# Performance work log

Measured on AMD Instinct MI355X. Metric: run time of the kernel, lower is better.

Reference implementation:

```python
import jax, jax.numpy as jnp
import numpy as np

HIDDEN = 768
HEADS = 12
HEAD_DIM = HIDDEN // HEADS


def setup_inputs() -> dict:
    key = jax.random.key(0)
    ks = jax.random.split(key, 5)
    B, S = 1, 4096
    scale = 1.0 / np.sqrt(HIDDEN)
    return {
        "x": jax.random.normal(ks[0], (B, S, HIDDEN), dtype=jnp.float32),
        "w_qkv": jax.random.normal(ks[1], (HIDDEN, 3 * HIDDEN), dtype=jnp.float32) * scale,
        "b_qkv": jnp.zeros((3 * HIDDEN,), dtype=jnp.float32),
        "w_proj": jax.random.normal(ks[2], (HIDDEN, HIDDEN), dtype=jnp.float32) * scale,
        "b_proj": jnp.zeros((HIDDEN,), dtype=jnp.float32),
    }


def reference(x, w_qkv, b_qkv, w_proj, b_proj):
    B, S, D = x.shape
    H, Hd = HEADS, HEAD_DIM
    qkv = x @ w_qkv + b_qkv                        # [B,S,3D]
    qkv = qkv.reshape(B, S, 3, H, Hd)
    q, k, v = (jnp.moveaxis(qkv[:, :, i], 2, 1) for i in range(3))  # [B,H,S,Hd]
    scale = 1.0 / np.sqrt(Hd)
    attn = jnp.einsum("bhqd,bhkd->bhqk", q, k) * scale
    attn = jax.nn.softmax(attn, axis=-1)
    o = jnp.einsum("bhqk,bhkd->bhqd", attn, v)     # [B,H,S,Hd]
    o = jnp.moveaxis(o, 1, 2).reshape(B, S, D)
    return o @ w_proj + b_proj
```

## Files before the change

kernel.cpp:

```cpp
#include <hip/hip_runtime.h>

#define S_LEN 4096
#define DMODEL 768
#define NHEAD 12
#define HDIM 64
#define DQKV 2304

typedef __attribute__((ext_vector_type(8))) __bf16 bf16x8;
typedef __attribute__((ext_vector_type(4))) float f32x4;
typedef __attribute__((ext_vector_type(8))) unsigned short ushort8;

#define LOG2E 1.4426950408889634f

#if __has_builtin(__builtin_amdgcn_exp2f)
#define EXP2(x) __builtin_amdgcn_exp2f(x)
#else
#define EXP2(x) exp2f(x)
#endif

static __device__ __forceinline__ unsigned short f2bf(float f) {
  unsigned int u = __float_as_uint(f);
  u += 0x7FFFu + ((u >> 16) & 1u);
  return (unsigned short)(u >> 16);
}

static __device__ __forceinline__ void gload_lds16(const unsigned short* g, unsigned short* l) {
  __builtin_amdgcn_global_load_lds(
      (const __attribute__((address_space(1))) unsigned int*)g,
      (__attribute__((address_space(3))) unsigned int*)l, 16, 0, 0);
}

__global__ __launch_bounds__(256) void k_prep(const float* __restrict__ x,
                                              const float* __restrict__ w_qkv,
                                              const float* __restrict__ w_proj,
                                              unsigned short* __restrict__ xb,
                                              unsigned short* __restrict__ wqkvT,
                                              unsigned short* __restrict__ wprojT) {
  __shared__ unsigned short t[64 * 65];
  int bid = blockIdx.x;
  int tid = threadIdx.x;
  if (bid < 1536) {
    int i = (bid * 256 + tid) * 8;
    const float4* p = reinterpret_cast<const float4*>(x + i);
    float4 a = p[0], b = p[1];
    ushort8 r;
    r[0] = f2bf(a.x); r[1] = f2bf(a.y); r[2] = f2bf(a.z); r[3] = f2bf(a.w);
    r[4] = f2bf(b.x); r[5] = f2bf(b.y); r[6] = f2bf(b.z); r[7] = f2bf(b.w);
    *reinterpret_cast<ushort8*>(xb + i) = r;
    return;
  }
  const float* in;
  unsigned short* out;
  int Kdim, Ndim, bx, by;
  if (bid < 1968) {
    int tt = bid - 1536;
    in = w_qkv; out = wqkvT; Kdim = DMODEL; Ndim = DQKV;
    bx = tt % 36; by = tt / 36;
  } else {
    int tt = bid - 1968;
    in = w_proj; out = wprojT; Kdim = DMODEL; Ndim = DMODEL;
    bx = tt % 12; by = tt / 12;
  }
  int k0 = by * 64, n0 = bx * 64;
#pragma unroll
  for (int p = 0; p < 4; ++p) {
    int r = p * 16 + (tid >> 4);
    int c = (tid & 15) * 4;
    float4 v = *reinterpret_cast<const float4*>(in + (size_t)(k0 + r) * Ndim + n0 + c);
    t[(c + 0) * 65 + r] = f2bf(v.x);
    t[(c + 1) * 65 + r] = f2bf(v.y);
    t[(c + 2) * 65 + r] = f2bf(v.z);
    t[(c + 3) * 65 + r] = f2bf(v.w);
  }
  __syncthreads();
#pragma unroll
  for (int p = 0; p < 2; ++p) {
    int task = p * 256 + tid;
    int rr = task >> 3;
    int cc = (task & 7) * 8;
    ushort8 r;
#pragma unroll
    for (int j = 0; j < 8; ++j) r[j] = t[rr * 65 + cc + j];
    *reinterpret_cast<ushort8*>(out + (size_t)(n0 + rr) * Kdim + k0 + cc) = r;
  }
}

__global__ __launch_bounds__(256) void k_gemm_qkv(const unsigned short* __restrict__ A,
                                                  const unsigned short* __restrict__ Bt,
                                                  const float* __restrict__ bias,
                                                  unsigned short* __restrict__ Qb,
                                                  unsigned short* __restrict__ Kf,
                                                  unsigned short* __restrict__ Vf) {
  __shared__ unsigned short As[2][128 * 32];
  __shared__ unsigned short Bs[2][96 * 32];

  int tid = threadIdx.x;
  int lane = tid & 63, wave = tid >> 6;
  int wr = wave >> 1, wc = wave & 1;
  int m0 = blockIdx.y * 128, n0 = blockIdx.x * 96;
  int r16 = lane & 15, g = lane >> 4;

  int ca0 = wave * 2, ca1 = wave * 2 + 1;
  int cb0 = (wave < 2) ? wave * 2 : wave + 2;
  int srow = lane >> 2, scol = (lane & 3) * 8;

  f32x4 acc[4][3] = {};

#define GSTAGE(BUF, K0)                                                                 \
  do {                                                                                  \
    gload_lds16(A + (size_t)(m0 + ca0 * 16 + srow) * DMODEL + (K0) + scol,              \
                &As[BUF][ca0 * 512]);                                                   \
    gload_lds16(A + (size_t)(m0 + ca1 * 16 + srow) * DMODEL + (K0) + scol,              \
                &As[BUF][ca1 * 512]);                                                   \
    gload_lds16(Bt + (size_t)(n0 + cb0 * 16 + srow) * DMODEL + (K0) + scol,             \
                &Bs[BUF][cb0 * 512]);                                                   \
    if (wave < 2)                                                                       \
      gload_lds16(Bt + (size_t)(n0 + (cb0 + 1) * 16 + srow) * DMODEL + (K0) + scol,     \
                  &Bs[BUF][(cb0 + 1) * 512]);                                           \
  } while (0)

  GSTAGE(0, 0);
  for (int kt = 0; kt < DMODEL / 32; ++kt) {
    int cur = kt & 1;
    __syncthreads();

    bf16x8 af[4], bfr[3];
#pragma unroll
    for (int m = 0; m < 4; ++m)
      af[m] = *reinterpret_cast<const bf16x8*>(&As[cur][(wr * 64 + m * 16 + r16) * 32 + g * 8]);
#pragma unroll
    for (int n = 0; n < 3; ++n)
      bfr[n] = *reinterpret_cast<const bf16x8*>(&Bs[cur][(wc * 48 + n * 16 + r16) * 32 + g * 8]);

    if (kt < DMODEL / 32 - 1) GSTAGE(cur ^ 1, (kt + 1) * 32);

#pragma unroll
    for (int m = 0; m < 4; ++m)
#pragma unroll
      for (int n = 0; n < 3; ++n)
        acc[m][n] = __builtin_amdgcn_mfma_f32_16x16x32_bf16(af[m], bfr[n], acc[m][n], 0, 0, 0);
  }
#undef GSTAGE

#pragma unroll
  for (int m = 0; m < 4; ++m) {
    int grow0 = m0 + wr * 64 + m * 16 + 4 * g;
#pragma unroll
    for (int n = 0; n < 3; ++n) {
      int gcol = n0 + wc * 48 + n * 16 + r16;
      float bv = bias[gcol];
      int sect = gcol / DMODEL;
      int rem = gcol - sect * DMODEL;
      int h = rem >> 6, hd = rem & 63;
      if (sect == 2) {
        int j = hd >> 4, r16v = hd & 15;
        int tile = grow0 >> 6, kk = (grow0 >> 5) & 1, g2 = (grow0 >> 3) & 3, e0 = grow0 & 7;
        size_t base = (((size_t)h * 64 + tile) * 8 + (j * 2 + kk)) * 512 +
                      (size_t)(g2 * 16 + r16v) * 8 + e0;
        ushort4 pk;
        pk.x = f2bf(acc[m][n][0] + bv);
        pk.y = f2bf(acc[m][n][1] + bv);
        pk.z = f2bf(acc[m][n][2] + bv);
        pk.w = f2bf(acc[m][n][3] + bv);
        *reinterpret_cast<ushort4*>(Vf + base) = pk;
      } else if (sect == 0) {
#pragma unroll
        for (int i = 0; i < 4; ++i)
          Qb[((size_t)h * S_LEN + grow0 + i) * HDIM + hd] =
              f2bf((acc[m][n][i] + bv) * (0.125f * LOG2E));
      } else {
        int kk = hd >> 5, g2 = (hd >> 3) & 3, e = hd & 7;
#pragma unroll
        for (int i = 0; i < 4; ++i) {
          int s = grow0 + i;
          int tile = s >> 6, r = s & 63;
          int j = (((r >> 2) & 1) << 1) | (r >> 5);
          int r16l = (r & 3) | (((r >> 3) & 3) << 2);
          size_t idx = (((size_t)h * 64 + tile) * 8 + (j * 2 + kk)) * 512 +
                       (size_t)(g2 * 16 + r16l) * 8 + e;
          Kf[idx] = f2bf(acc[m][n][i] + bv);
        }
      }
    }
  }
}

__global__ __launch_bounds__(256) void k_gemm_proj(const unsigned short* __restrict__ A,
                                                   const unsigned short* __restrict__ Bt,
                                                   const float* __restrict__ bias,
                                                   float* __restrict__ outf) {
  __shared__ unsigned short As[2][64 * 32];
  __shared__ unsigned short Bs[2][64 * 32];

  int tid = threadIdx.x;
  int lane = tid & 63, wave = tid >> 6;
  int wr = wave >> 1, wc = wave & 1;
  int m0 = blockIdx.y * 64, n0 = blockIdx.x * 64;
  int r16 = lane & 15, g = lane >> 4;
  int srow = lane >> 2, scol = (lane & 3) * 8;

  f32x4 acc[2][2] = {};

#define GSTAGE(BUF, K0)                                                                 \
  do {                                                                                  \
    gload_lds16(A + (size_t)(m0 + wave * 16 + srow) * DMODEL + (K0) + scol,             \
                &As[BUF][wave * 512]);                                                  \
    gload_lds16(Bt + (size_t)(n0 + wave * 16 + srow) * DMODEL + (K0) + scol,            \
                &Bs[BUF][wave * 512]);                                                  \
  } while (0)

  GSTAGE(0, 0);
  for (int kt = 0; kt < DMODEL / 32; ++kt) {
    int cur = kt & 1;
    __syncthreads();

    bf16x8 af[2], bfr[2];
#pragma unroll
    for (int m = 0; m < 2; ++m)
      af[m] = *reinterpret_cast<const bf16x8*>(&As[cur][(wr * 32 + m * 16 + r16) * 32 + g * 8]);
#pragma unroll
    for (int n = 0; n < 2; ++n)
      bfr[n] = *reinterpret_cast<const bf16x8*>(&Bs[cur][(wc * 32 + n * 16 + r16) * 32 + g * 8]);

    if (kt < DMODEL / 32 - 1) GSTAGE(cur ^ 1, (kt + 1) * 32);

#pragma unroll
    for (int m = 0; m < 2; ++m)
#pragma unroll
      for (int n = 0; n < 2; ++n)
        acc[m][n] = __builtin_amdgcn_mfma_f32_16x16x32_bf16(af[m], bfr[n], acc[m][n], 0, 0, 0);
  }
#undef GSTAGE

#pragma unroll
  for (int m = 0; m < 2; ++m) {
    int grow0 = m0 + wr * 32 + m * 16 + 4 * g;
#pragma unroll
    for (int n = 0; n < 2; ++n) {
      int gcol = n0 + wc * 32 + n * 16 + r16;
      float bv = bias[gcol];
#pragma unroll
      for (int i = 0; i < 4; ++i)
        outf[(size_t)(grow0 + i) * DMODEL + gcol] = acc[m][n][i] + bv;
    }
  }
}

__global__ __launch_bounds__(256, 3) void k_attn(const unsigned short* __restrict__ Q,
                                                 const unsigned short* __restrict__ Kf,
                                                 const unsigned short* __restrict__ Vf,
                                                 float* __restrict__ Opart,
                                                 float* __restrict__ Lpart) {
  __shared__ unsigned short ldsK[2][4096];
  __shared__ unsigned short ldsV[2][4096];

  int tid = threadIdx.x;
  int lane = tid & 63, wave = tid >> 6;
  int r16 = lane & 15, g = lane >> 4;

  int bid = blockIdx.x;
  int gid = (bid & 7) * 96 + (bid >> 3);
  int h = gid >> 6;
  int rem = gid & 63;
  int half = rem & 1;
  int qb = rem >> 1;
  int qbaseA = qb * 128 + wave * 16;
  int qbaseB = qbaseA + 64;
  int tb = half * 32;

  const unsigned short* KfH = Kf + (size_t)h * (64 * 4096);
  const unsigned short* VfH = Vf + (size_t)h * (64 * 4096);
  float* OpH = Opart + ((size_t)half * NHEAD + h) * S_LEN * HDIM;
  float* LpH = Lpart + ((size_t)half * NHEAD + h) * S_LEN;

  const unsigned short* qpA = Q + ((size_t)h * S_LEN + qbaseA + r16) * HDIM + g * 8;
  const unsigned short* qpB = Q + ((size_t)h * S_LEN + qbaseB + r16) * HDIM + g * 8;
  bf16x8 qf0a = *reinterpret_cast<const bf16x8*>(qpA);
  bf16x8 qf1a = *reinterpret_cast<const bf16x8*>(qpA + 32);
  bf16x8 qf0b = *reinterpret_cast<const bf16x8*>(qpB);
  bf16x8 qf1b = *reinterpret_cast<const bf16x8*>(qpB + 32);

  f32x4 oaccA[4] = {}, oaccB[4] = {};
  f32x4 lsumA = {}, lsumB = {};
  bf16x8 bones;
#pragma unroll
  for (int e = 0; e < 8; ++e) bones[e] = (__bf16)1.0f;

  int c0 = wave, c1 = wave + 4;

#define STAGE(BUF, T)                                                        \
  do {                                                                       \
    const unsigned short* kg_ = KfH + (size_t)(T) * 4096;                    \
    const unsigned short* vg_ = VfH + (size_t)(T) * 4096;                    \
    gload_lds16(kg_ + c0 * 512 + lane * 8, &ldsK[BUF][c0 * 512]);            \
    gload_lds16(kg_ + c1 * 512 + lane * 8, &ldsK[BUF][c1 * 512]);            \
    gload_lds16(vg_ + c0 * 512 + lane * 8, &ldsV[BUF][c0 * 512]);            \
    gload_lds16(vg_ + c1 * 512 + lane * 8, &ldsV[BUF][c1 * 512]);            \
  } while (0)

#define QK(SARR, QF0, QF1)                                                              \
  do {                                                                                  \
    _Pragma("unroll") for (int j_ = 0; j_ < 4; ++j_) {                                  \
      f32x4 z_ = {};                                                                    \
      z_ = __builtin_amdgcn_mfma_f32_16x16x32_bf16(kfr_[2 * j_], QF0, z_, 0, 0, 0);     \
      SARR[j_] = __builtin_amdgcn_mfma_f32_16x16x32_bf16(kfr_[2 * j_ + 1], QF1, z_, 0, 0, 0); \
    }                                                                                   \
  } while (0)

#define SOFTPV(SARR, LSUM, OACC)                                                        \
  do {                                                                                  \
    float p_[4][4];                                                                     \
    _Pragma("unroll") for (int j_ = 0; j_ < 4; ++j_)                                    \
      _Pragma("unroll") for (int i_ = 0; i_ < 4; ++i_)                                  \
        p_[j_][i_] = EXP2(SARR[j_][i_]);                                                \
    bf16x8 pa0_, pa1_;                                                                  \
    _Pragma("unroll") for (int e_ = 0; e_ < 8; ++e_) {                                  \
      pa0_[e_] = (__bf16)p_[2 * (e_ >> 2)][e_ & 3];                                     \
      pa1_[e_] = (__bf16)p_[1 + 2 * (e_ >> 2)][e_ & 3];                                 \
    }                                                                                   \
    LSUM = __builtin_amdgcn_mfma_f32_16x16x32_bf16(pa0_, bones, LSUM, 0, 0, 0);         \
    LSUM = __builtin_amdgcn_mfma_f32_16x16x32_bf16(pa1_, bones, LSUM, 0, 0, 0);         \
    _Pragma("unroll") for (int j_ = 0; j_ < 4; ++j_) {                                  \
      OACC[j_] = __builtin_amdgcn_mfma_f32_16x16x32_bf16(pa0_, vfr_[2 * j_], OACC[j_], 0, 0, 0); \
      OACC[j_] = __builtin_amdgcn_mfma_f32_16x16x32_bf16(pa1_, vfr_[2 * j_ + 1], OACC[j_], 0, 0, 0); \
    }                                                                                   \
  } while (0)

#define BODY(CUR, DO_STAGE, T)                                                          \
  do {                                                                                  \
    __syncthreads();                                                                    \
    bf16x8 kfr_[8], vfr_[8];                                                            \
    _Pragma("unroll") for (int f_ = 0; f_ < 8; ++f_) {                                  \
      kfr_[f_] = *reinterpret_cast<const bf16x8*>(&ldsK[CUR][f_ * 512 + lane * 8]);     \
      vfr_[f_] = *reinterpret_cast<const bf16x8*>(&ldsV[CUR][f_ * 512 + lane * 8]);     \
    }                                                                                   \
    if (DO_STAGE) STAGE((CUR) ^ 1, (T) + 1);                                            \
    f32x4 sA_[4], sB_[4];                                                               \
    QK(sA_, qf0a, qf1a);                                                                \
    QK(sB_, qf0b, qf1b);                                                                \
    SOFTPV(sA_, lsumA, oaccA);                                                          \
    SOFTPV(sB_, lsumB, oaccB);                                                          \
  } while (0)

  STAGE(0, tb);
  BODY(0, true, tb);
  for (int pr = 0; pr < 15; ++pr) {
    BODY(1, true, tb + 2 * pr + 1);
    BODY(0, true, tb + 2 * pr + 2);
  }
  BODY(1, false, tb + 31);
#undef BODY
#undef SOFTPV
#undef QK
#undef STAGE

#pragma unroll
  for (int i = 0; i < 4; ++i) {
    int srowA = qbaseA + 4 * g + i;
    int srowB = qbaseB + 4 * g + i;
#pragma unroll
    for (int j = 0; j < 4; ++j) {
      int col = j * 16 + r16;
      OpH[(size_t)srowA * HDIM + col] = oaccA[j][i];
      OpH[(size_t)srowB * HDIM + col] = oaccB[j][i];
    }
  }
  if (r16 == 0) {
#pragma unroll
    for (int i = 0; i < 4; ++i) {
      LpH[qbaseA + 4 * g + i] = lsumA[i];
      LpH[qbaseB + 4 * g + i] = lsumB[i];
    }
  }
}

__global__ __launch_bounds__(256) void k_combine(const float* __restrict__ Opart,
                                                 const float* __restrict__ Lpart,
                                                 unsigned short* __restrict__ O) {
  int gidx = blockIdx.x * 256 + threadIdx.x;
  int h = gidx >> 15;
  int rem = gidx & 32767;
  int s = rem >> 3;
  int d0 = (rem & 7) * 8;
  size_t i0 = (size_t)h * S_LEN + s;
  size_t o0 = i0 * HDIM + d0;
  const size_t HS_O = (size_t)NHEAD * S_LEN * HDIM;
  const size_t HS_L = (size_t)NHEAD * S_LEN;

  float l0 = Lpart[i0], l1 = Lpart[HS_L + i0];
  float inv = 1.0f / (l0 + l1);
  float4 a0 = *reinterpret_cast<const float4*>(Opart + o0);
  float4 a1 = *reinterpret_cast<const float4*>(Opart + o0 + 4);
  float4 b0 = *reinterpret_cast<const float4*>(Opart + HS_O + o0);
  float4 b1 = *reinterpret_cast<const float4*>(Opart + HS_O + o0 + 4);
  ushort8 r;
  r[0] = f2bf((a0.x + b0.x) * inv);
  r[1] = f2bf((a0.y + b0.y) * inv);
  r[2] = f2bf((a0.z + b0.z) * inv);
  r[3] = f2bf((a0.w + b0.w) * inv);
  r[4] = f2bf((a1.x + b1.x) * inv);
  r[5] = f2bf((a1.y + b1.y) * inv);
  r[6] = f2bf((a1.z + b1.z) * inv);
  r[7] = f2bf((a1.w + b1.w) * inv);
  *reinterpret_cast<ushort8*>(O + (size_t)s * DMODEL + h * HDIM + d0) = r;
}

extern "C" void kernel_launch(void* const* d_in, const int* in_sizes, int n_in,
                              void* d_out, int out_size, void* d_ws, size_t ws_size,
                              hipStream_t stream) {
  const float* x = (const float*)d_in[0];
  const float* w_qkv = (const float*)d_in[1];
  const float* b_qkv = (const float*)d_in[2];
  const float* w_proj = (const float*)d_in[3];
  const float* b_proj = (const float*)d_in[4];
  float* out = (float*)d_out;

  unsigned short* ws16 = (unsigned short*)d_ws;
  unsigned short* xb = ws16;
  unsigned short* wqkvT = xb + (size_t)S_LEN * DMODEL;
  unsigned short* wprojT = wqkvT + (size_t)DQKV * DMODEL;
  unsigned short* Qb = wprojT + (size_t)DMODEL * DMODEL;
  unsigned short* Kf = Qb + (size_t)NHEAD * S_LEN * HDIM;
  unsigned short* Vf = Kf + (size_t)NHEAD * S_LEN * HDIM;
  float* Opart = (float*)(Vf + (size_t)NHEAD * S_LEN * HDIM);
  float* Lpart = Opart + (size_t)2 * NHEAD * S_LEN * HDIM;
  unsigned short* Ob = xb;

  k_prep<<<2112, 256, 0, stream>>>(x, w_qkv, w_proj, xb, wqkvT, wprojT);
  k_gemm_qkv<<<dim3(DQKV / 96, S_LEN / 128), 256, 0, stream>>>(xb, wqkvT, b_qkv, Qb, Kf, Vf);
  k_attn<<<768, 256, 0, stream>>>(Qb, Kf, Vf, Opart, Lpart);
  k_combine<<<(NHEAD * S_LEN * 8) / 256, 256, 0, stream>>>(Opart, Lpart, Ob);
  k_gemm_proj<<<dim3(DMODEL / 64, S_LEN / 64), 256, 0, stream>>>(Ob, wprojT, b_proj, out);
}
```

Measured before the change: 110.9 us.

## Fuse split-KV combine into projection GEMM A-operand loading

Removes the separate combine kernel and instead has the projection GEMM read fp32 partial attention outputs and partial sums directly, normalizing and converting to bf16 while staging the A tile into LDS. The aim is to save a kernel launch and the round trip of the bf16 intermediate through global memory. In exchange, every column block re-reads and re-normalizes the fp32 partials, which multiplies A-side traffic and ALU work. The register-staged A load also replaces the async LDS load.

New measurement: 122.9 us. +10.8%, slower.

```diff
diff --git a/kernel.cpp b/kernel.cpp
--- a/kernel.cpp
+++ b/kernel.cpp
@@ -185,7 +185,8 @@
   }
 }
 
-__global__ __launch_bounds__(256) void k_gemm_proj(const unsigned short* __restrict__ A,
+__global__ __launch_bounds__(256) void k_gemm_proj(const float* __restrict__ Opart,
+                                                   const float* __restrict__ Lpart,
                                                    const unsigned short* __restrict__ Bt,
                                                    const float* __restrict__ bias,
                                                    float* __restrict__ outf) {
@@ -198,18 +199,50 @@
   int m0 = blockIdx.y * 64, n0 = blockIdx.x * 64;
   int r16 = lane & 15, g = lane >> 4;
   int srow = lane >> 2, scol = (lane & 3) * 8;
+  int s = m0 + wave * 16 + srow;
+
+  const size_t HS_O = (size_t)NHEAD * S_LEN * HDIM;
+  const size_t HS_L = (size_t)NHEAD * S_LEN;
 
   f32x4 acc[2][2] = {};
-
-#define GSTAGE(BUF, K0)                                                                 \
-  do {                                                                                  \
-    gload_lds16(A + (size_t)(m0 + wave * 16 + srow) * DMODEL + (K0) + scol,             \
-                &As[BUF][wave * 512]);                                                  \
-    gload_lds16(Bt + (size_t)(n0 + wave * 16 + srow) * DMODEL + (K0) + scol,            \
-                &Bs[BUF][wave * 512]);                                                  \
-  } while (0)
-
-  GSTAGE(0, 0);
+  float4 a0_, a1_, b0_, b1_;
+  float l_;
+
+#define BSTAGE(BUF, K0)                                                                \
+  gload_lds16(Bt + (size_t)(n0 + wave * 16 + srow) * DMODEL + (K0) + scol,             \
+              &Bs[BUF][wave * 512])
+
+#define ALOAD(K0)                                                                      \
+  do {                                                                                 \
+    int h_ = (K0) >> 6;                                                                \
+    int d_ = ((K0) & 63) + scol;                                                       \
+    size_t base_ = ((size_t)h_ * S_LEN + s) * HDIM + d_;                               \
+    a0_ = *reinterpret_cast<const float4*>(Opart + base_);                             \
+    a1_ = *reinterpret_cast<const float4*>(Opart + base_ + 4);                         \
+    b0_ = *reinterpret_cast<const float4*>(Opart + HS_O + base_);                      \
+    b1_ = *reinterpret_cast<const float4*>(Opart + HS_O + base_ + 4);                  \
+    l_ = Lpart[(size_t)h_ * S_LEN + s] + Lpart[HS_L + (size_t)h_ * S_LEN + s];         \
+  } while (0)
+
+#define AWRITE(BUF)                                                                    \
+  do {                                                                                 \
+    float inv_ = 1.0f / l_;                                                            \
+    ushort8 w_;                                                                        \
+    w_[0] = f2bf((a0_.x + b0_.x) * inv_);                                              \
+    w_[1] = f2bf((a0_.y + b0_.y) * inv_);                                              \
+    w_[2] = f2bf((a0_.z + b0_.z) * inv_);                                              \
+    w_[3] = f2bf((a0_.w + b0_.w) * inv_);                                              \
+    w_[4] = f2bf((a1_.x + b1_.x) * inv_);                                              \
+    w_[5] = f2bf((a1_.y + b1_.y) * inv_);                                              \
+    w_[6] = f2bf((a1_.z + b1_.z) * inv_);                                              \
+    w_[7] = f2bf((a1_.w + b1_.w) * inv_);                                              \
+    *reinterpret_cast<ushort8*>(&As[BUF][wave * 512 + lane * 8]) = w_;                 \
+  } while (0)
+
+  ALOAD(0);
+  BSTAGE(0, 0);
+  AWRITE(0);
+
   for (int kt = 0; kt < DMODEL / 32; ++kt) {
     int cur = kt & 1;
     __syncthreads();
@@ -222,15 +255,22 @@
     for (int n = 0; n < 2; ++n)
       bfr[n] = *reinterpret_cast<const bf16x8*>(&Bs[cur][(wc * 32 + n * 16 + r16) * 32 + g * 8]);
 
-    if (kt < DMODEL / 32 - 1) GSTAGE(cur ^ 1, (kt + 1) * 32);
+    if (kt < DMODEL / 32 - 1) {
+      ALOAD((kt + 1) * 32);
+      BSTAGE(cur ^ 1, (kt + 1) * 32);
+    }
 
 #pragma unroll
     for (int m = 0; m < 2; ++m)
 #pragma unroll
       for (int n = 0; n < 2; ++n)
         acc[m][n] = __builtin_amdgcn_mfma_f32_16x16x32_bf16(af[m], bfr[n], acc[m][n], 0, 0, 0);
-  }
-#undef GSTAGE
+
+    if (kt < DMODEL / 32 - 1) AWRITE(cur ^ 1);
+  }
+#undef BSTAGE
+#undef ALOAD
+#undef AWRITE
 
 #pragma unroll
   for (int m = 0; m < 2; ++m) {
@@ -374,37 +414,6 @@
   }
 }
 
-__global__ __launch_bounds__(256) void k_combine(const float* __restrict__ Opart,
-                                                 const float* __restrict__ Lpart,
-                                                 unsigned short* __restrict__ O) {
-  int gidx = blockIdx.x * 256 + threadIdx.x;
-  int h = gidx >> 15;
-  int rem = gidx & 32767;
-  int s = rem >> 3;
-  int d0 = (rem & 7) * 8;
-  size_t i0 = (size_t)h * S_LEN + s;
-  size_t o0 = i0 * HDIM + d0;
-  const size_t HS_O = (size_t)NHEAD * S_LEN * HDIM;
-  const size_t HS_L = (size_t)NHEAD * S_LEN;
-
-  float l0 = Lpart[i0], l1 = Lpart[HS_L + i0];
-  float inv = 1.0f / (l0 + l1);
-  float4 a0 = *reinterpret_cast<const float4*>(Opart + o0);
-  float4 a1 = *reinterpret_cast<const float4*>(Opart + o0 + 4);
-  float4 b0 = *reinterpret_cast<const float4*>(Opart + HS_O + o0);
-  float4 b1 = *reinterpret_cast<const float4*>(Opart + HS_O + o0 + 4);
-  ushort8 r;
-  r[0] = f2bf((a0.x + b0.x) * inv);
-  r[1] = f2bf((a0.y + b0.y) * inv);
-  r[2] = f2bf((a0.z + b0.z) * inv);
-  r[3] = f2bf((a0.w + b0.w) * inv);
-  r[4] = f2bf((a1.x + b1.x) * inv);
-  r[5] = f2bf((a1.y + b1.y) * inv);
-  r[6] = f2bf((a1.z + b1.z) * inv);
-  r[7] = f2bf((a1.w + b1.w) * inv);
-  *reinterpret_cast<ushort8*>(O + (size_t)s * DMODEL + h * HDIM + d0) = r;
-}
-
 extern "C" void kernel_launch(void* const* d_in, const int* in_sizes, int n_in,
                               void* d_out, int out_size, void* d_ws, size_t ws_size,
                               hipStream_t stream) {
@@ -424,11 +433,9 @@
   unsigned short* Vf = Kf + (size_t)NHEAD * S_LEN * HDIM;
   float* Opart = (float*)(Vf + (size_t)NHEAD * S_LEN * HDIM);
   float* Lpart = Opart + (size_t)2 * NHEAD * S_LEN * HDIM;
-  unsigned short* Ob = xb;
 
   k_prep<<<2112, 256, 0, stream>>>(x, w_qkv, w_proj, xb, wqkvT, wprojT);
   k_gemm_qkv<<<dim3(DQKV / 96, S_LEN / 128), 256, 0, stream>>>(xb, wqkvT, b_qkv, Qb, Kf, Vf);
   k_attn<<<768, 256, 0, stream>>>(Qb, Kf, Vf, Opart, Lpart);
-  k_combine<<<(NHEAD * S_LEN * 8) / 256, 256, 0, stream>>>(Opart, Lpart, Ob);
-  k_gemm_proj<<<dim3(DMODEL / 64, S_LEN / 64), 256, 0, stream>>>(Ob, wprojT, b_proj, out);
-}
+  k_gemm_proj<<<dim3(DMODEL / 64, S_LEN / 64), 256, 0, stream>>>(Opart, Lpart, wprojT, b_proj, out);
+}
```
